# Kernel tuning notes

Hardware: AMD Instinct MI355X
Metric: run time of the kernel (lower is better)

## Reference

```python
import jax, jax.numpy as jnp
import numpy as np

P = 1048576   # total sampled points
N = 8192      # rays
E = 8         # experts
H = 128       # expert hidden dim
TOP_K = 2
INTERVAL = 0.5      # stepsize * voxel_size_ratio
ACT_SHIFT = -4.0    # models[-1].act_shift
THRESH = 1e-4       # fast_color_thres (ndc=False)


def raw2alpha(d):
    # Raw2Alpha: alpha = 1 - exp(-softplus(density + act_shift) * interval)
    return 1.0 - jnp.exp(-jax.nn.softplus(d + ACT_SHIFT) * INTERVAL)


def alphas2weights(alpha, ray_id, n_rays):
    # Sequential per-ray transmittance: w_j = alpha_j * prod_{k<j in ray}(1 - alpha_k)
    la = jnp.log1p(-jnp.clip(alpha, 0.0, 1.0 - 1e-6))      # [P], <= 0
    cum = jnp.cumsum(la)
    excl = cum - la                                          # exclusive cumsum, nonincreasing
    # offset per ray = excl at first point of the (sorted) segment == segment max
    offset = jax.ops.segment_max(excl, ray_id, num_segments=n_rays)
    T = jnp.exp(excl - offset[ray_id])                       # transmittance before each point
    weights = alpha * T
    alphainv_last = jnp.exp(jax.ops.segment_sum(la, ray_id, num_segments=n_rays))
    return weights, alphainv_last


def setup_inputs() -> dict:
    key = jax.random.key(0)
    ks = jax.random.split(key, 12)
    s = 0.3  # weight scale keeping activations in a sane range
    return {
        "ray_pts": jax.random.uniform(ks[0], (P, 3), dtype=jnp.float32),
        "viewdirs": jax.random.normal(ks[1], (N, 3), dtype=jnp.float32),
        "bg": jnp.ones((3,), dtype=jnp.float32),
        "Wd1": jax.random.normal(ks[2], (3, H), dtype=jnp.float32) * s,
        "bd1": jnp.zeros((H,), dtype=jnp.float32),
        "Wd2": jax.random.normal(ks[3], (H, 1), dtype=jnp.float32) * s,
        "Wg": jax.random.normal(ks[4], (6, E), dtype=jnp.float32) * s,
        "We1": jax.random.normal(ks[5], (E, 6, H), dtype=jnp.float32) * s,
        "be1": jnp.zeros((E, H), dtype=jnp.float32),
        "Wrgb": jax.random.normal(ks[6], (E, H, 3), dtype=jnp.float32) * s,
        "Walpha": jax.random.normal(ks[7], (E, H, 1), dtype=jnp.float32) * s,
        "ray_id": jnp.sort(jax.random.randint(ks[8], (P,), 0, N)).astype(jnp.int32),
    }


def reference(ray_pts, viewdirs, bg, Wd1, bd1, Wd2, Wg, We1, be1, Wrgb, Walpha, ray_id):
    # --- density grid query + activation ---
    hd = jax.nn.relu(ray_pts @ Wd1 + bd1)                    # [P,H]
    density = (hd @ Wd2)[:, 0]                               # [P]
    alpha0 = raw2alpha(density)
    # filter low density (zeroing alpha == dropping the point from the cumprod)
    alpha0 = jnp.where(alpha0 > THRESH, alpha0, 0.0)
    w0, _ = alphas2weights(alpha0, ray_id, N)
    # filter low transmittance (w0 <= THRESH also covers alpha0 == 0)
    keep = w0 > THRESH                                        # [P] bool

    # --- gate: softmax over experts, top-k, renormalize ---
    x = jnp.concatenate([ray_pts, viewdirs[ray_id]], axis=-1)  # [P,6]
    probs = jax.nn.softmax(x @ Wg, axis=-1)                    # [P,E]
    vals, idx = jax.lax.top_k(probs, TOP_K)                    # [P,K]
    vals = vals / jnp.sum(vals, axis=-1, keepdims=True)        # top_k > 1
    g = jnp.sum(vals[..., None] * jax.nn.one_hot(idx, E, dtype=vals.dtype), axis=1)  # [P,E]
    g = g * keep[:, None].astype(g.dtype)

    # --- per-expert radiance / alpha, mixed by gate weights ---
    rgb = jnp.zeros((ray_pts.shape[0], 3), dtype=ray_pts.dtype)
    alpha_mix = jnp.zeros((ray_pts.shape[0],), dtype=ray_pts.dtype)
    for e in range(E):  # fixed small expert count
        h = jax.nn.relu(x @ We1[e] + be1[e])                   # [P,H]
        rgb_e = jax.nn.sigmoid(h @ Wrgb[e])                    # [P,3]
        a_e = raw2alpha((h @ Walpha[e])[:, 0])                 # [P]
        rgb = rgb + g[:, e:e + 1] * rgb_e
        alpha_mix = alpha_mix + g[:, e] * a_e

    # --- composite: Alphas2Weights + segment_coo sum + background ---
    w, alphainv_last = alphas2weights(alpha_mix, ray_id, N)
    rgb_marched = jax.ops.segment_sum(w[:, None] * rgb, ray_id, num_segments=N)
    rgb_marched = rgb_marched + alphainv_last[:, None] * bg
    return rgb_marched
```

## Files before the change

kernel.cpp:

```cpp
#include <hip/hip_runtime.h>

#define PTOT   1048576
#define NRAYS  8192
#define THRESH 1e-4f

typedef float F2 __attribute__((ext_vector_type(2)));

__device__ __forceinline__ F2 f2splat(float s){ F2 r; r.x = s; r.y = s; return r; }
__device__ __forceinline__ F2 f2fma(F2 a, float b, F2 c){
    return __builtin_elementwise_fma(a, f2splat(b), c);
}
__device__ __forceinline__ float raw2alpha_f(float d){
    return 1.0f - rsqrtf(1.0f + __expf(d - 4.0f));
}

__global__ __launch_bounds__(256) void k_point(
    const float* __restrict__ pts, const float* __restrict__ vdirs,
    const int* __restrict__ ray_id,
    const float* __restrict__ Wd1, const float* __restrict__ bd1,
    const float* __restrict__ Wd2, const float* __restrict__ Wg,
    float* __restrict__ alpha0, float* __restrict__ g0a, int* __restrict__ eea,
    float4* __restrict__ vd, int* __restrict__ ray_off)
{
    __shared__ float4 WD4[128];
    __shared__ float  WD2s[128];
    __shared__ float  WGs[8][6];
    int t = threadIdx.x;
    if (t < 128){
        WD4[t] = make_float4(Wd1[t], Wd1[128+t], Wd1[256+t], bd1[t]);
        WD2s[t] = Wd2[t];
    }
    if (t < 48) WGs[t & 7][t >> 3] = Wg[t];
    __syncthreads();

    int base = blockIdx.x * 2048 + t;
    F2 px[4], py[4], pz[4], vx[4], vy[4], vz[4], dens[4];
    int rid0[4], rid1[4];
    #pragma unroll
    for (int q=0;q<4;q++){
        int p0 = base + (2*q)*256, p1 = p0 + 256;
        px[q] = (F2){pts[3*p0],   pts[3*p1]};
        py[q] = (F2){pts[3*p0+1], pts[3*p1+1]};
        pz[q] = (F2){pts[3*p0+2], pts[3*p1+2]};
        int r0 = ray_id[p0], r1 = ray_id[p1];
        rid0[q] = r0; rid1[q] = r1;
        vx[q] = (F2){vdirs[3*r0],   vdirs[3*r1]};
        vy[q] = (F2){vdirs[3*r0+1], vdirs[3*r1+1]};
        vz[q] = (F2){vdirs[3*r0+2], vdirs[3*r1+2]};
        dens[q] = f2splat(0.f);
    }
    #pragma unroll
    for (int q=0;q<4;q++){
        int p0 = base + (2*q)*256, p1 = p0 + 256;
        vd[p0] = make_float4(vx[q].x, vy[q].x, vz[q].x, 0.f);
        vd[p1] = make_float4(vx[q].y, vy[q].y, vz[q].y, 0.f);
        int prev0 = (p0 == 0) ? -1 : ray_id[p0-1];
        if (prev0 != rid0[q]) for (int r=prev0+1; r<=rid0[q]; ++r) ray_off[r] = p0;
        int prev1 = ray_id[p1-1];
        if (prev1 != rid1[q]) for (int r=prev1+1; r<=rid1[q]; ++r) ray_off[r] = p1;
        if (p1 == PTOT-1) for (int r=rid1[q]+1; r<=NRAYS; ++r) ray_off[r] = PTOT;
    }
    #pragma unroll 2
    for (int i=0;i<128;i++){
        float4 w = WD4[i]; float w2 = WD2s[i];
        #pragma unroll
        for (int q=0;q<4;q++){
            F2 h = f2fma(px[q], w.x, f2fma(py[q], w.y, f2fma(pz[q], w.z, f2splat(w.w))));
            h = __builtin_elementwise_max(h, f2splat(0.f));
            dens[q] = f2fma(h, w2, dens[q]);
        }
    }
    #pragma unroll
    for (int q=0;q<4;q++){
        float a0 = raw2alpha_f(dens[q].x);
        float a1 = raw2alpha_f(dens[q].y);
        alpha0[base + (2*q)*256]   = (a0 > THRESH) ? a0 : 0.f;
        alpha0[base + (2*q+1)*256] = (a1 > THRESH) ? a1 : 0.f;
    }
    float m0[8], m1[8]; int i0[8], i1[8];
    #pragma unroll
    for (int j=0;j<8;j++){ m0[j]=-3.0e38f; m1[j]=-3.0e38f; i0[j]=0; i1[j]=0; }
    for (int e=0;e<8;e++){
        float w0=WGs[e][0],w1=WGs[e][1],w2=WGs[e][2],w3=WGs[e][3],w4=WGs[e][4],w5=WGs[e][5];
        #pragma unroll
        for (int q=0;q<4;q++){
            F2 l = f2fma(px[q],w0, f2fma(py[q],w1, f2fma(pz[q],w2,
                   f2fma(vx[q],w3, f2fma(vy[q],w4,
                   __builtin_elementwise_fma(vz[q], f2splat(w5), f2splat(0.f)))))));
            int j0 = 2*q, j1 = 2*q+1;
            float lx = l.x, ly = l.y;
            if (lx > m0[j0]){ m1[j0]=m0[j0]; i1[j0]=i0[j0]; m0[j0]=lx; i0[j0]=e; }
            else if (lx > m1[j0]){ m1[j0]=lx; i1[j0]=e; }
            if (ly > m0[j1]){ m1[j1]=m0[j1]; i1[j1]=i0[j1]; m0[j1]=ly; i0[j1]=e; }
            else if (ly > m1[j1]){ m1[j1]=ly; i1[j1]=e; }
        }
    }
    #pragma unroll
    for (int j=0;j<8;j++){
        float g0 = __fdividef(1.0f, 1.0f + __expf(m1[j]-m0[j]));
        g0a[base + j*256] = g0;
        eea[base + j*256] = i0[j] | (i1[j] << 8);
    }
}

__global__ __launch_bounds__(256) void k_scan0(const float* __restrict__ alpha0,
                                               const int* __restrict__ eea,
                                               const int* __restrict__ ray_off,
                                               unsigned char* __restrict__ keep,
                                               int* __restrict__ cntA)
{
    __shared__ int wcs[4][8];
    int t = threadIdx.x, lane = t & 63, w = t >> 6;
    int wid = blockIdx.x*4 + w;
    int c[8];
    #pragma unroll
    for (int e=0;e<8;e++) c[e]=0;
    int s = ray_off[wid], e = ray_off[wid+1];
    float carry = 1.f;
    for (int ch = s; ch < e; ch += 64){
        int p = ch + lane;
        bool in = p < e;
        float a = in ? alpha0[p] : 0.f;
        int  ee = in ? eea[p] : 0;
        float incl = 1.f - a;
        #pragma unroll
        for (int d=1; d<64; d<<=1){ float tt = __shfl_up(incl, d); if (lane >= d) incl *= tt; }
        float excl = __shfl_up(incl, 1); if (lane == 0) excl = 1.f;
        float w0 = a * carry * excl;
        int k = (in && w0 > THRESH) ? 1 : 0;
        if (in) keep[p] = (unsigned char)k;
        int e0 = ee & 255, e1 = (ee >> 8) & 255;
        #pragma unroll
        for (int x=0;x<8;x++){
            unsigned long long m0 = __ballot(k && e0==x);
            unsigned long long m1 = __ballot(k && e1==x);
            c[x] += __popcll(m0) + __popcll(m1);
        }
        carry *= __shfl(incl, 63);
    }
    if (lane == 0){
        #pragma unroll
        for (int x=0;x<8;x++) wcs[w][x] = c[x];
    }
    __syncthreads();
    if (t < 8){
        int sum = wcs[0][t]+wcs[1][t]+wcs[2][t]+wcs[3][t];
        if (sum) atomicAdd(&cntA[t], sum);
    }
}

__global__ __launch_bounds__(256) void k_fill(const unsigned char* __restrict__ keep,
                                              const float* __restrict__ g0a,
                                              const int* __restrict__ eea,
                                              const int* __restrict__ cntA,
                                              int* __restrict__ curA,
                                              int2* __restrict__ ent)
{
    __shared__ int wc[4][8];
    __shared__ int wb[4][8];
    __shared__ int sOff[8];
    int t = threadIdx.x, lane = t & 63, w = t >> 6;
    unsigned long long lt = (1ull << lane) - 1ull;
    int base = blockIdx.x * 2048;

    int c[8];
    #pragma unroll
    for (int e=0;e<8;e++) c[e]=0;
    for (int j=0;j<8;j++){
        int p = base + (j*4 + w)*64 + lane;
        int k = keep[p];
        int ee = eea[p];
        int e0 = ee & 255, e1 = (ee >> 8) & 255;
        #pragma unroll
        for (int e=0;e<8;e++){
            unsigned long long m0 = __ballot(k && e0==e);
            unsigned long long m1 = __ballot(k && e1==e);
            c[e] += __popcll(m0) + __popcll(m1);
        }
    }
    if (lane == 0){
        #pragma unroll
        for (int e=0;e<8;e++) wc[w][e] = c[e];
    }
    if (t == 0){
        int acc = 0;
        for (int e=0;e<8;e++){ sOff[e] = acc; acc += cntA[e]; }
    }
    __syncthreads();
    if (t < 8){
        int tot = wc[0][t]+wc[1][t]+wc[2][t]+wc[3][t];
        int b = sOff[t] + (tot ? atomicAdd(&curA[t], tot) : 0);
        wb[0][t] = b; b += wc[0][t];
        wb[1][t] = b; b += wc[1][t];
        wb[2][t] = b; b += wc[2][t];
        wb[3][t] = b;
    }
    __syncthreads();

    int cur[8];
    #pragma unroll
    for (int e=0;e<8;e++) cur[e] = wb[w][e];
    for (int j=0;j<8;j++){
        int p = base + (j*4 + w)*64 + lane;
        int k = keep[p];
        float g0 = g0a[p];
        int ee = eea[p];
        int e0 = ee & 255, e1 = (ee >> 8) & 255;
        #pragma unroll
        for (int e=0;e<8;e++){
            unsigned long long m0 = __ballot(k && e0==e);
            unsigned long long m1 = __ballot(k && e1==e);
            if (k && e0==e)
                ent[cur[e] + __popcll(m0 & lt)] = make_int2(p, __float_as_int(g0));
            if (k && e1==e)
                ent[cur[e] + __popcll(m0) + __popcll(m1 & lt)] =
                    make_int2(p | (1 << 30), __float_as_int(1.0f - g0));
            cur[e] += __popcll(m0) + __popcll(m1);
        }
    }
}

__global__ __launch_bounds__(256) void k_expert(
    const int2* __restrict__ ent, const int* __restrict__ cntA,
    const float* __restrict__ pts, const float4* __restrict__ vd,
    const float* __restrict__ We1, const float* __restrict__ be1,
    const float* __restrict__ Wrgb, const float* __restrict__ Walpha,
    float4* __restrict__ res)
{
    int e    = blockIdx.x >> 9;
    int bi   = blockIdx.x & 511;
    int base = bi * 2048;

    __shared__ float4 WA[128];
    __shared__ float4 WB[128];
    __shared__ float4 WC[128];
    __shared__ int sSeg[2];
    int t = threadIdx.x;
    if (t < 128){
        const float* w = We1 + e*768;
        WA[t] = make_float4(w[t], w[128+t], w[256+t], w[384+t]);
        WB[t] = make_float4(w[512+t], w[640+t], be1[e*128+t], Walpha[e*128+t]);
        const float* wr = Wrgb + e*384 + 3*t;
        WC[t] = make_float4(wr[0], wr[1], wr[2], 0.f);
    }
    if (t == 0){
        int acc = 0;
        for (int i=0;i<e;i++) acc += cntA[i];
        sSeg[0] = acc; sSeg[1] = cntA[e];
    }
    __syncthreads();
    int n = sSeg[1];
    if (base >= n) return;
    const int2* eb = ent + sSeg[0];

    F2 x0[4],x1[4],x2[4],x3[4],x4[4],x5[4];
    F2 ar[4],ag[4],ab[4],aa[4];
    #pragma unroll
    for (int pr=0;pr<4;pr++){
        int idx0 = base + t + (2*pr)*256, idx1 = idx0 + 256;
        int2 r0 = (idx0 < n) ? eb[idx0] : make_int2(0,0);
        int2 r1 = (idx1 < n) ? eb[idx1] : make_int2(0,0);
        int p0 = r0.x & 0x0FFFFFFF, p1 = r1.x & 0x0FFFFFFF;
        x0[pr] = (F2){pts[3*p0],   pts[3*p1]};
        x1[pr] = (F2){pts[3*p0+1], pts[3*p1+1]};
        x2[pr] = (F2){pts[3*p0+2], pts[3*p1+2]};
        float4 v0 = vd[p0], v1 = vd[p1];
        x3[pr] = (F2){v0.x, v1.x};
        x4[pr] = (F2){v0.y, v1.y};
        x5[pr] = (F2){v0.z, v1.z};
        ar[pr] = f2splat(0.f); ag[pr] = f2splat(0.f);
        ab[pr] = f2splat(0.f); aa[pr] = f2splat(0.f);
    }
    #pragma unroll 2
    for (int i=0;i<128;i++){
        float4 wa = WA[i], wb = WB[i], wc = WC[i];
        #pragma unroll
        for (int pr=0;pr<4;pr++){
            F2 h = f2fma(x0[pr],wa.x, f2fma(x1[pr],wa.y, f2fma(x2[pr],wa.z,
                   f2fma(x3[pr],wa.w, f2fma(x4[pr],wb.x, f2fma(x5[pr],wb.y,
                   f2splat(wb.z)))))));
            h = __builtin_elementwise_max(h, f2splat(0.f));
            ar[pr] = f2fma(h, wc.x, ar[pr]);
            ag[pr] = f2fma(h, wc.y, ag[pr]);
            ab[pr] = f2fma(h, wc.z, ab[pr]);
            aa[pr] = f2fma(h, wb.w, aa[pr]);
        }
    }
    #pragma unroll
    for (int pr=0;pr<4;pr++){
        #pragma unroll
        for (int sel=0; sel<2; sel++){
            int idx = base + t + (2*pr+sel)*256;
            if (idx < n){
                int2 rec = eb[idx];
                float vr = sel ? ar[pr].y : ar[pr].x;
                float vg = sel ? ag[pr].y : ag[pr].x;
                float vb = sel ? ab[pr].y : ab[pr].x;
                float va = sel ? aa[pr].y : aa[pr].x;
                float sr = __fdividef(1.0f, 1.0f + __expf(-vr));
                float sg = __fdividef(1.0f, 1.0f + __expf(-vg));
                float sb = __fdividef(1.0f, 1.0f + __expf(-vb));
                float a  = raw2alpha_f(va);
                float g  = __int_as_float(rec.y);
                int pp   = rec.x & 0x0FFFFFFF;
                int slot = ((unsigned)rec.x) >> 30;
                res[2*(size_t)pp + slot] = make_float4(g*sr, g*sg, g*sb, g*a);
            }
        }
    }
}

__global__ __launch_bounds__(256) void k_scan1(const float4* __restrict__ res,
                                               const unsigned char* __restrict__ keep,
                                               const int* __restrict__ ray_off,
                                               const float* __restrict__ bg,
                                               float* __restrict__ out)
{
    int wid  = (blockIdx.x*blockDim.x + threadIdx.x) >> 6;
    int lane = threadIdx.x & 63;
    if (wid >= NRAYS) return;
    int s = ray_off[wid], e = ray_off[wid+1];
    float carry = 1.f;
    float accx = 0.f, accy = 0.f, accz = 0.f;
    for (int c = s; c < e; c += 64){
        int p = c + lane;
        float4 v = make_float4(0.f,0.f,0.f,0.f);
        if (p < e && keep[p]){
            float4 v0 = res[2*(size_t)p];
            float4 v1 = res[2*(size_t)p + 1];
            v = make_float4(v0.x+v1.x, v0.y+v1.y, v0.z+v1.z, v0.w+v1.w);
        }
        float a = v.w;
        float incl = 1.f - a;
        #pragma unroll
        for (int d=1; d<64; d<<=1){ float tt = __shfl_up(incl, d); if (lane >= d) incl *= tt; }
        float excl = __shfl_up(incl, 1); if (lane == 0) excl = 1.f;
        float w = a * carry * excl;
        accx = fmaf(w, v.x, accx);
        accy = fmaf(w, v.y, accy);
        accz = fmaf(w, v.z, accz);
        carry *= __shfl(incl, 63);
    }
    #pragma unroll
    for (int d=32; d; d>>=1){
        accx += __shfl_xor(accx, d);
        accy += __shfl_xor(accy, d);
        accz += __shfl_xor(accz, d);
    }
    if (lane == 0){
        out[3*wid+0] = accx + carry*bg[0];
        out[3*wid+1] = accy + carry*bg[1];
        out[3*wid+2] = accz + carry*bg[2];
    }
}

extern "C" void kernel_launch(void* const* d_in, const int* in_sizes, int n_in,
                              void* d_out, int out_size, void* d_ws, size_t ws_size,
                              hipStream_t stream)
{
    const float* pts    = (const float*)d_in[0];
    const float* vdirs  = (const float*)d_in[1];
    const float* bg     = (const float*)d_in[2];
    const float* Wd1    = (const float*)d_in[3];
    const float* bd1    = (const float*)d_in[4];
    const float* Wd2    = (const float*)d_in[5];
    const float* Wg     = (const float*)d_in[6];
    const float* We1    = (const float*)d_in[7];
    const float* be1    = (const float*)d_in[8];
    const float* Wrgb   = (const float*)d_in[9];
    const float* Walpha = (const float*)d_in[10];
    const int*   ray_id = (const int*)d_in[11];
    float* out = (float*)d_out;

    char* ws = (char*)d_ws;
    size_t off = 0;
    float* alpha0        = (float*)(ws + off); off += (size_t)PTOT*4;
    float* g0a           = (float*)(ws + off); off += (size_t)PTOT*4;
    int*   eea           = (int*)  (ws + off); off += (size_t)PTOT*4;
    unsigned char* keep  = (unsigned char*)(ws + off); off += (size_t)PTOT;
    int*   ray_off       = (int*)  (ws + off); off += 33024;
    int*   cntA          = (int*)  (ws + off); off += 256;
    int*   curA          = (int*)  (ws + off); off += 256;
    off = (off + 255) & ~(size_t)255;
    float4* vd           = (float4*)(ws + off); off += (size_t)PTOT*16;
    int2*  ent           = (int2*) (ws + off); off += (size_t)2*PTOT*8;
    float4* res          = (float4*)(ws + off); off += ((size_t)2*PTOT+2)*16;

    hipMemsetAsync(cntA, 0, 512, stream);

    k_point <<<PTOT/2048, 256, 0, stream>>>(pts, vdirs, ray_id, Wd1, bd1, Wd2, Wg,
                                            alpha0, g0a, eea, vd, ray_off);
    k_scan0 <<<NRAYS/4, 256, 0, stream>>>(alpha0, eea, ray_off, keep, cntA);
    k_fill  <<<PTOT/2048, 256, 0, stream>>>(keep, g0a, eea, cntA, curA, ent);
    k_expert<<<8*512, 256, 0, stream>>>(ent, cntA, pts, vd,
                                        We1, be1, Wrgb, Walpha, res);
    k_scan1 <<<NRAYS*64/256, 256, 0, stream>>>(res, keep, ray_off, bg, out);
}
```

Before: 249.1 us.

## Fuse five phase kernels into one cooperative persistent kernel with grid syncs

Merges the point, scan, fill, expert and composite kernels into one cooperative kernel of 512 persistent blocks separated by grid-wide syncs. This removes the memset and the per-launch gaps between kernels. The expert phase now walks 2048-aligned padded segments through a flat chunk loop instead of launching 8×512 mostly-empty blocks. It keeps a fallback path of separate launches if the cooperative launch fails. The risks are grid-sync overhead, lower parallelism in the expert phase, and block-count limits imposed by occupancy.

```diff
diff --git a/kernel.cpp b/kernel.cpp
--- a/kernel.cpp
+++ b/kernel.cpp
@@ -1,8 +1,12 @@
 #include <hip/hip_runtime.h>
+#include <hip/hip_cooperative_groups.h>
+
+namespace cg = cooperative_groups;
 
 #define PTOT   1048576
 #define NRAYS  8192
 #define THRESH 1e-4f
+#define NBLK   512
 
 typedef float F2 __attribute__((ext_vector_type(2)));
 
@@ -14,26 +18,27 @@
     return 1.0f - rsqrtf(1.0f + __expf(d - 4.0f));
 }
 
-__global__ __launch_bounds__(256) void k_point(
+
+__device__ __forceinline__ void phase1(int bid, int t,
     const float* __restrict__ pts, const float* __restrict__ vdirs,
     const int* __restrict__ ray_id,
     const float* __restrict__ Wd1, const float* __restrict__ bd1,
     const float* __restrict__ Wd2, const float* __restrict__ Wg,
     float* __restrict__ alpha0, float* __restrict__ g0a, int* __restrict__ eea,
-    float4* __restrict__ vd, int* __restrict__ ray_off)
-{
-    __shared__ float4 WD4[128];
+    float4* __restrict__ vd, int* __restrict__ ray_off, int* __restrict__ cc)
+{
+    __shared__ float4 WD4s[128];
     __shared__ float  WD2s[128];
     __shared__ float  WGs[8][6];
-    int t = threadIdx.x;
     if (t < 128){
-        WD4[t] = make_float4(Wd1[t], Wd1[128+t], Wd1[256+t], bd1[t]);
+        WD4s[t] = make_float4(Wd1[t], Wd1[128+t], Wd1[256+t], bd1[t]);
         WD2s[t] = Wd2[t];
     }
     if (t < 48) WGs[t & 7][t >> 3] = Wg[t];
+    if (bid == 0 && t < 16) cc[t] = 0;
     __syncthreads();
 
-    int base = blockIdx.x * 2048 + t;
+    int base = bid * 2048 + t;
     F2 px[4], py[4], pz[4], vx[4], vy[4], vz[4], dens[4];
     int rid0[4], rid1[4];
     #pragma unroll
@@ -62,10 +67,10 @@
     }
     #pragma unroll 2
     for (int i=0;i<128;i++){
-        float4 w = WD4[i]; float w2 = WD2s[i];
+        float4 wv = WD4s[i]; float w2 = WD2s[i];
         #pragma unroll
         for (int q=0;q<4;q++){
-            F2 h = f2fma(px[q], w.x, f2fma(py[q], w.y, f2fma(pz[q], w.z, f2splat(w.w))));
+            F2 h = f2fma(px[q], wv.x, f2fma(py[q], wv.y, f2fma(pz[q], wv.z, f2splat(wv.w))));
             h = __builtin_elementwise_max(h, f2splat(0.f));
             dens[q] = f2fma(h, w2, dens[q]);
         }
@@ -103,40 +108,41 @@
     }
 }
 
-__global__ __launch_bounds__(256) void k_scan0(const float* __restrict__ alpha0,
-                                               const int* __restrict__ eea,
-                                               const int* __restrict__ ray_off,
-                                               unsigned char* __restrict__ keep,
-                                               int* __restrict__ cntA)
+__device__ __forceinline__ void phase2(int bid, int t,
+    const float* __restrict__ alpha0, const int* __restrict__ eea,
+    const int* __restrict__ ray_off,
+    unsigned char* __restrict__ keep, int* __restrict__ cc)
 {
     __shared__ int wcs[4][8];
-    int t = threadIdx.x, lane = t & 63, w = t >> 6;
-    int wid = blockIdx.x*4 + w;
+    int lane = t & 63, w = t >> 6;
     int c[8];
     #pragma unroll
     for (int e=0;e<8;e++) c[e]=0;
-    int s = ray_off[wid], e = ray_off[wid+1];
-    float carry = 1.f;
-    for (int ch = s; ch < e; ch += 64){
-        int p = ch + lane;
-        bool in = p < e;
-        float a = in ? alpha0[p] : 0.f;
-        int  ee = in ? eea[p] : 0;
-        float incl = 1.f - a;
-        #pragma unroll
-        for (int d=1; d<64; d<<=1){ float tt = __shfl_up(incl, d); if (lane >= d) incl *= tt; }
-        float excl = __shfl_up(incl, 1); if (lane == 0) excl = 1.f;
-        float w0 = a * carry * excl;
-        int k = (in && w0 > THRESH) ? 1 : 0;
-        if (in) keep[p] = (unsigned char)k;
-        int e0 = ee & 255, e1 = (ee >> 8) & 255;
-        #pragma unroll
-        for (int x=0;x<8;x++){
-            unsigned long long m0 = __ballot(k && e0==x);
-            unsigned long long m1 = __ballot(k && e1==x);
-            c[x] += __popcll(m0) + __popcll(m1);
-        }
-        carry *= __shfl(incl, 63);
+    for (int rr=0; rr<4; rr++){
+        int wid = bid*4 + w + rr*2048;
+        int s = ray_off[wid], e = ray_off[wid+1];
+        float carry = 1.f;
+        for (int ch = s; ch < e; ch += 64){
+            int p = ch + lane;
+            bool in = p < e;
+            float a = in ? alpha0[p] : 0.f;
+            int  ee = in ? eea[p] : 0;
+            float incl = 1.f - a;
+            #pragma unroll
+            for (int d=1; d<64; d<<=1){ float tt = __shfl_up(incl, d); if (lane >= d) incl *= tt; }
+            float excl = __shfl_up(incl, 1); if (lane == 0) excl = 1.f;
+            float w0 = a * carry * excl;
+            int k = (in && w0 > THRESH) ? 1 : 0;
+            if (in) keep[p] = (unsigned char)k;
+            int e0 = ee & 255, e1 = (ee >> 8) & 255;
+            #pragma unroll
+            for (int x=0;x<8;x++){
+                unsigned long long m0 = __ballot(k && e0==x);
+                unsigned long long m1 = __ballot(k && e1==x);
+                c[x] += __popcll(m0) + __popcll(m1);
+            }
+            carry *= __shfl(incl, 63);
+        }
     }
     if (lane == 0){
         #pragma unroll
@@ -145,23 +151,21 @@
     __syncthreads();
     if (t < 8){
         int sum = wcs[0][t]+wcs[1][t]+wcs[2][t]+wcs[3][t];
-        if (sum) atomicAdd(&cntA[t], sum);
-    }
-}
-
-__global__ __launch_bounds__(256) void k_fill(const unsigned char* __restrict__ keep,
-                                              const float* __restrict__ g0a,
-                                              const int* __restrict__ eea,
-                                              const int* __restrict__ cntA,
-                                              int* __restrict__ curA,
-                                              int2* __restrict__ ent)
-{
-    __shared__ int wc[4][8];
-    __shared__ int wb[4][8];
-    __shared__ int sOff[8];
-    int t = threadIdx.x, lane = t & 63, w = t >> 6;
+        if (sum) atomicAdd(&cc[t], sum);
+    }
+}
+
+__device__ __forceinline__ void phase3(int bid, int t,
+    const unsigned char* __restrict__ keep, const float* __restrict__ g0a,
+    const int* __restrict__ eea, int* __restrict__ cc, int2* __restrict__ ent)
+{
+    __shared__ int wc3[4][8];
+    __shared__ int wb3[4][8];
+    __shared__ int sOff3[8];
+    int lane = t & 63, w = t >> 6;
     unsigned long long lt = (1ull << lane) - 1ull;
-    int base = blockIdx.x * 2048;
+    int base = bid * 2048;
+    int* cntA = cc; int* curA = cc + 8;
 
     int c[8];
     #pragma unroll
@@ -180,26 +184,26 @@
     }
     if (lane == 0){
         #pragma unroll
-        for (int e=0;e<8;e++) wc[w][e] = c[e];
+        for (int e=0;e<8;e++) wc3[w][e] = c[e];
     }
     if (t == 0){
         int acc = 0;
-        for (int e=0;e<8;e++){ sOff[e] = acc; acc += cntA[e]; }
+        for (int e=0;e<8;e++){ sOff3[e] = acc; acc += (cntA[e] + 2047) & ~2047; }
     }
     __syncthreads();
     if (t < 8){
-        int tot = wc[0][t]+wc[1][t]+wc[2][t]+wc[3][t];
-        int b = sOff[t] + (tot ? atomicAdd(&curA[t], tot) : 0);
-        wb[0][t] = b; b += wc[0][t];
-        wb[1][t] = b; b += wc[1][t];
-        wb[2][t] = b; b += wc[2][t];
-        wb[3][t] = b;
+        int tot = wc3[0][t]+wc3[1][t]+wc3[2][t]+wc3[3][t];
+        int b = sOff3[t] + (tot ? atomicAdd(&curA[t], tot) : 0);
+        wb3[0][t] = b; b += wc3[0][t];
+        wb3[1][t] = b; b += wc3[1][t];
+        wb3[2][t] = b; b += wc3[2][t];
+        wb3[3][t] = b;
     }
     __syncthreads();
 
     int cur[8];
     #pragma unroll
-    for (int e=0;e<8;e++) cur[e] = wb[w][e];
+    for (int e=0;e<8;e++) cur[e] = wb3[w][e];
     for (int j=0;j<8;j++){
         int p = base + (j*4 + w)*64 + lane;
         int k = keep[p];
@@ -220,139 +224,198 @@
     }
 }
 
-__global__ __launch_bounds__(256) void k_expert(
-    const int2* __restrict__ ent, const int* __restrict__ cntA,
+__device__ __forceinline__ void phase4(int bid, int t,
     const float* __restrict__ pts, const float4* __restrict__ vd,
     const float* __restrict__ We1, const float* __restrict__ be1,
     const float* __restrict__ Wrgb, const float* __restrict__ Walpha,
+    const int* __restrict__ cc, const int2* __restrict__ ent,
     float4* __restrict__ res)
 {
-    int e    = blockIdx.x >> 9;
-    int bi   = blockIdx.x & 511;
-    int base = bi * 2048;
-
-    __shared__ float4 WA[128];
-    __shared__ float4 WB[128];
-    __shared__ float4 WC[128];
-    __shared__ int sSeg[2];
-    int t = threadIdx.x;
-    if (t < 128){
-        const float* w = We1 + e*768;
-        WA[t] = make_float4(w[t], w[128+t], w[256+t], w[384+t]);
-        WB[t] = make_float4(w[512+t], w[640+t], be1[e*128+t], Walpha[e*128+t]);
-        const float* wr = Wrgb + e*384 + 3*t;
-        WC[t] = make_float4(wr[0], wr[1], wr[2], 0.f);
-    }
-    if (t == 0){
+    __shared__ float4 WA[128], WB[128], WC[128];
+    int cnt8[8], offP[8];
+    {
         int acc = 0;
-        for (int i=0;i<e;i++) acc += cntA[i];
-        sSeg[0] = acc; sSeg[1] = cntA[e];
-    }
-    __syncthreads();
-    int n = sSeg[1];
-    if (base >= n) return;
-    const int2* eb = ent + sSeg[0];
-
-    F2 x0[4],x1[4],x2[4],x3[4],x4[4],x5[4];
-    F2 ar[4],ag[4],ab[4],aa[4];
-    #pragma unroll
-    for (int pr=0;pr<4;pr++){
-        int idx0 = base + t + (2*pr)*256, idx1 = idx0 + 256;
-        int2 r0 = (idx0 < n) ? eb[idx0] : make_int2(0,0);
-        int2 r1 = (idx1 < n) ? eb[idx1] : make_int2(0,0);
-        int p0 = r0.x & 0x0FFFFFFF, p1 = r1.x & 0x0FFFFFFF;
-        x0[pr] = (F2){pts[3*p0],   pts[3*p1]};
-        x1[pr] = (F2){pts[3*p0+1], pts[3*p1+1]};
-        x2[pr] = (F2){pts[3*p0+2], pts[3*p1+2]};
-        float4 v0 = vd[p0], v1 = vd[p1];
-        x3[pr] = (F2){v0.x, v1.x};
-        x4[pr] = (F2){v0.y, v1.y};
-        x5[pr] = (F2){v0.z, v1.z};
-        ar[pr] = f2splat(0.f); ag[pr] = f2splat(0.f);
-        ab[pr] = f2splat(0.f); aa[pr] = f2splat(0.f);
-    }
-    #pragma unroll 2
-    for (int i=0;i<128;i++){
-        float4 wa = WA[i], wb = WB[i], wc = WC[i];
+        #pragma unroll
+        for (int x=0;x<8;x++){ cnt8[x]=cc[x]; offP[x]=acc; acc += (cnt8[x]+2047)&~2047; }
+    }
+    int lastck = (offP[7] + cnt8[7] - 1) >> 11;
+    for (int ck = bid; ck <= lastck; ck += NBLK){
+        int e = -1, base = 0;
+        #pragma unroll
+        for (int x=0;x<8;x++){
+            int bx = (ck << 11) - offP[x];
+            if (bx >= 0 && bx < cnt8[x]){ e = x; base = bx; }
+        }
+        if (e < 0) continue;
+        __syncthreads();
+        if (t < 128){
+            const float* wp = We1 + e*768;
+            WA[t] = make_float4(wp[t], wp[128+t], wp[256+t], wp[384+t]);
+            WB[t] = make_float4(wp[512+t], wp[640+t], be1[e*128+t], Walpha[e*128+t]);
+            const float* wr = Wrgb + e*384 + 3*t;
+            WC[t] = make_float4(wr[0], wr[1], wr[2], 0.f);
+        }
+        __syncthreads();
+        int n = cnt8[e];
+        const int2* eb = ent + offP[e];
+
+        F2 x0[4],x1[4],x2[4],x3[4],x4[4],x5[4];
+        F2 ar[4],ag[4],ab[4],aa[4];
         #pragma unroll
         for (int pr=0;pr<4;pr++){
-            F2 h = f2fma(x0[pr],wa.x, f2fma(x1[pr],wa.y, f2fma(x2[pr],wa.z,
-                   f2fma(x3[pr],wa.w, f2fma(x4[pr],wb.x, f2fma(x5[pr],wb.y,
-                   f2splat(wb.z)))))));
-            h = __builtin_elementwise_max(h, f2splat(0.f));
-            ar[pr] = f2fma(h, wc.x, ar[pr]);
-            ag[pr] = f2fma(h, wc.y, ag[pr]);
-            ab[pr] = f2fma(h, wc.z, ab[pr]);
-            aa[pr] = f2fma(h, wb.w, aa[pr]);
-        }
-    }
-    #pragma unroll
-    for (int pr=0;pr<4;pr++){
-        #pragma unroll
-        for (int sel=0; sel<2; sel++){
-            int idx = base + t + (2*pr+sel)*256;
-            if (idx < n){
-                int2 rec = eb[idx];
-                float vr = sel ? ar[pr].y : ar[pr].x;
-                float vg = sel ? ag[pr].y : ag[pr].x;
-                float vb = sel ? ab[pr].y : ab[pr].x;
-                float va = sel ? aa[pr].y : aa[pr].x;
-                float sr = __fdividef(1.0f, 1.0f + __expf(-vr));
-                float sg = __fdividef(1.0f, 1.0f + __expf(-vg));
-                float sb = __fdividef(1.0f, 1.0f + __expf(-vb));
-                float a  = raw2alpha_f(va);
-                float g  = __int_as_float(rec.y);
-                int pp   = rec.x & 0x0FFFFFFF;
-                int slot = ((unsigned)rec.x) >> 30;
-                res[2*(size_t)pp + slot] = make_float4(g*sr, g*sg, g*sb, g*a);
+            int idx0 = base + t + (2*pr)*256, idx1 = idx0 + 256;
+            int2 r0 = (idx0 < n) ? eb[idx0] : make_int2(0,0);
+            int2 r1 = (idx1 < n) ? eb[idx1] : make_int2(0,0);
+            int p0 = r0.x & 0x0FFFFFFF, p1 = r1.x & 0x0FFFFFFF;
+            x0[pr] = (F2){pts[3*p0],   pts[3*p1]};
+            x1[pr] = (F2){pts[3*p0+1], pts[3*p1+1]};
+            x2[pr] = (F2){pts[3*p0+2], pts[3*p1+2]};
+            float4 v0 = vd[p0], v1 = vd[p1];
+            x3[pr] = (F2){v0.x, v1.x};
+            x4[pr] = (F2){v0.y, v1.y};
+            x5[pr] = (F2){v0.z, v1.z};
+            ar[pr] = f2splat(0.f); ag[pr] = f2splat(0.f);
+            ab[pr] = f2splat(0.f); aa[pr] = f2splat(0.f);
+        }
+        #pragma unroll 2
+        for (int i=0;i<128;i++){
+            float4 wa = WA[i], wb = WB[i], wc = WC[i];
+            #pragma unroll
+            for (int pr=0;pr<4;pr++){
+                F2 h = f2fma(x0[pr],wa.x, f2fma(x1[pr],wa.y, f2fma(x2[pr],wa.z,
+                       f2fma(x3[pr],wa.w, f2fma(x4[pr],wb.x, f2fma(x5[pr],wb.y,
+                       f2splat(wb.z)))))));
+                h = __builtin_elementwise_max(h, f2splat(0.f));
+                ar[pr] = f2fma(h, wc.x, ar[pr]);
+                ag[pr] = f2fma(h, wc.y, ag[pr]);
+                ab[pr] = f2fma(h, wc.z, ab[pr]);
+                aa[pr] = f2fma(h, wb.w, aa[pr]);
             }
         }
-    }
-}
-
-__global__ __launch_bounds__(256) void k_scan1(const float4* __restrict__ res,
-                                               const unsigned char* __restrict__ keep,
-                                               const int* __restrict__ ray_off,
-                                               const float* __restrict__ bg,
-                                               float* __restrict__ out)
-{
-    int wid  = (blockIdx.x*blockDim.x + threadIdx.x) >> 6;
-    int lane = threadIdx.x & 63;
-    if (wid >= NRAYS) return;
-    int s = ray_off[wid], e = ray_off[wid+1];
-    float carry = 1.f;
-    float accx = 0.f, accy = 0.f, accz = 0.f;
-    for (int c = s; c < e; c += 64){
-        int p = c + lane;
-        float4 v = make_float4(0.f,0.f,0.f,0.f);
-        if (p < e && keep[p]){
-            float4 v0 = res[2*(size_t)p];
-            float4 v1 = res[2*(size_t)p + 1];
-            v = make_float4(v0.x+v1.x, v0.y+v1.y, v0.z+v1.z, v0.w+v1.w);
-        }
-        float a = v.w;
-        float incl = 1.f - a;
-        #pragma unroll
-        for (int d=1; d<64; d<<=1){ float tt = __shfl_up(incl, d); if (lane >= d) incl *= tt; }
-        float excl = __shfl_up(incl, 1); if (lane == 0) excl = 1.f;
-        float w = a * carry * excl;
-        accx = fmaf(w, v.x, accx);
-        accy = fmaf(w, v.y, accy);
-        accz = fmaf(w, v.z, accz);
-        carry *= __shfl(incl, 63);
-    }
-    #pragma unroll
-    for (int d=32; d; d>>=1){
-        accx += __shfl_xor(accx, d);
-        accy += __shfl_xor(accy, d);
-        accz += __shfl_xor(accz, d);
-    }
-    if (lane == 0){
-        out[3*wid+0] = accx + carry*bg[0];
-        out[3*wid+1] = accy + carry*bg[1];
-        out[3*wid+2] = accz + carry*bg[2];
-    }
-}
+        #pragma unroll
+        for (int pr=0;pr<4;pr++){
+            #pragma unroll
+            for (int sel=0; sel<2; sel++){
+                int idx = base + t + (2*pr+sel)*256;
+                if (idx < n){
+                    int2 rec = eb[idx];
+                    float vr = sel ? ar[pr].y : ar[pr].x;
+                    float vg = sel ? ag[pr].y : ag[pr].x;
+                    float vb = sel ? ab[pr].y : ab[pr].x;
+                    float va = sel ? aa[pr].y : aa[pr].x;
+                    float sr = __fdividef(1.0f, 1.0f + __expf(-vr));
+                    float sg = __fdividef(1.0f, 1.0f + __expf(-vg));
+                    float sb = __fdividef(1.0f, 1.0f + __expf(-vb));
+                    float a  = raw2alpha_f(va);
+                    float g  = __int_as_float(rec.y);
+                    int pp   = rec.x & 0x0FFFFFFF;
+                    int slot = ((unsigned)rec.x) >> 30;
+                    res[2*(size_t)pp + slot] = make_float4(g*sr, g*sg, g*sb, g*a);
+                }
+            }
+        }
+    }
+}
+
+__device__ __forceinline__ void phase5(int bid, int t,
+    const float4* __restrict__ res, const unsigned char* __restrict__ keep,
+    const int* __restrict__ ray_off, const float* __restrict__ bg,
+    float* __restrict__ out)
+{
+    int lane = t & 63, w = t >> 6;
+    for (int rr=0; rr<4; rr++){
+        int wid = bid*4 + w + rr*2048;
+        int s = ray_off[wid], e = ray_off[wid+1];
+        float carry = 1.f;
+        float accx = 0.f, accy = 0.f, accz = 0.f;
+        for (int c = s; c < e; c += 64){
+            int p = c + lane;
+            float4 v = make_float4(0.f,0.f,0.f,0.f);
+            if (p < e && keep[p]){
+                float4 v0 = res[2*(size_t)p];
+                float4 v1 = res[2*(size_t)p + 1];
+                v = make_float4(v0.x+v1.x, v0.y+v1.y, v0.z+v1.z, v0.w+v1.w);
+            }
+            float a = v.w;
+            float incl = 1.f - a;
+            #pragma unroll
+            for (int d=1; d<64; d<<=1){ float tt = __shfl_up(incl, d); if (lane >= d) incl *= tt; }
+            float excl = __shfl_up(incl, 1); if (lane == 0) excl = 1.f;
+            float wgt = a * carry * excl;
+            accx = fmaf(wgt, v.x, accx);
+            accy = fmaf(wgt, v.y, accy);
+            accz = fmaf(wgt, v.z, accz);
+            carry *= __shfl(incl, 63);
+        }
+        #pragma unroll
+        for (int d=32; d; d>>=1){
+            accx += __shfl_xor(accx, d);
+            accy += __shfl_xor(accy, d);
+            accz += __shfl_xor(accz, d);
+        }
+        if (lane == 0){
+            out[3*wid+0] = accx + carry*bg[0];
+            out[3*wid+1] = accy + carry*bg[1];
+            out[3*wid+2] = accz + carry*bg[2];
+        }
+    }
+}
+
+__global__ __launch_bounds__(256, 2) void k_mega(
+    const float* __restrict__ pts, const float* __restrict__ vdirs,
+    const float* __restrict__ bg,
+    const float* __restrict__ Wd1, const float* __restrict__ bd1,
+    const float* __restrict__ Wd2, const float* __restrict__ Wg,
+    const float* __restrict__ We1, const float* __restrict__ be1,
+    const float* __restrict__ Wrgb, const float* __restrict__ Walpha,
+    const int* __restrict__ ray_id,
+    float* __restrict__ out,
+    float* __restrict__ alpha0, float* __restrict__ g0a, int* __restrict__ eea,
+    unsigned char* __restrict__ keep, int* __restrict__ ray_off,
+    int* __restrict__ cc, float4* __restrict__ vd,
+    int2* __restrict__ ent, float4* __restrict__ res)
+{
+    cg::grid_group gg = cg::this_grid();
+    int bid = blockIdx.x, t = threadIdx.x;
+    phase1(bid, t, pts, vdirs, ray_id, Wd1, bd1, Wd2, Wg,
+           alpha0, g0a, eea, vd, ray_off, cc);
+    gg.sync();
+    phase2(bid, t, alpha0, eea, ray_off, keep, cc);
+    gg.sync();
+    phase3(bid, t, keep, g0a, eea, cc, ent);
+    gg.sync();
+    phase4(bid, t, pts, vd, We1, be1, Wrgb, Walpha, cc, ent, res);
+    gg.sync();
+    phase5(bid, t, res, keep, ray_off, bg, out);
+}
+
+__global__ __launch_bounds__(256) void k_p1(
+    const float* pts, const float* vdirs, const int* ray_id,
+    const float* Wd1, const float* bd1, const float* Wd2, const float* Wg,
+    float* alpha0, float* g0a, int* eea, float4* vd, int* ray_off, int* cc)
+{ phase1(blockIdx.x, threadIdx.x, pts, vdirs, ray_id, Wd1, bd1, Wd2, Wg,
+         alpha0, g0a, eea, vd, ray_off, cc); }
+
+__global__ __launch_bounds__(256) void k_p2(
+    const float* alpha0, const int* eea, const int* ray_off,
+    unsigned char* keep, int* cc)
+{ phase2(blockIdx.x, threadIdx.x, alpha0, eea, ray_off, keep, cc); }
+
+__global__ __launch_bounds__(256) void k_p3(
+    const unsigned char* keep, const float* g0a, const int* eea,
+    int* cc, int2* ent)
+{ phase3(blockIdx.x, threadIdx.x, keep, g0a, eea, cc, ent); }
+
+__global__ __launch_bounds__(256) void k_p4(
+    const float* pts, const float4* vd,
+    const float* We1, const float* be1, const float* Wrgb, const float* Walpha,
+    const int* cc, const int2* ent, float4* res)
+{ phase4(blockIdx.x, threadIdx.x, pts, vd, We1, be1, Wrgb, Walpha, cc, ent, res); }
+
+__global__ __launch_bounds__(256) void k_p5(
+    const float4* res, const unsigned char* keep, const int* ray_off,
+    const float* bg, float* out)
+{ phase5(blockIdx.x, threadIdx.x, res, keep, ray_off, bg, out); }
 
 extern "C" void kernel_launch(void* const* d_in, const int* in_sizes, int n_in,
                               void* d_out, int out_size, void* d_ws, size_t ws_size,
@@ -379,20 +442,27 @@
     int*   eea           = (int*)  (ws + off); off += (size_t)PTOT*4;
     unsigned char* keep  = (unsigned char*)(ws + off); off += (size_t)PTOT;
     int*   ray_off       = (int*)  (ws + off); off += 33024;
-    int*   cntA          = (int*)  (ws + off); off += 256;
-    int*   curA          = (int*)  (ws + off); off += 256;
+    int*   cc            = (int*)  (ws + off); off += 256;
     off = (off + 255) & ~(size_t)255;
     float4* vd           = (float4*)(ws + off); off += (size_t)PTOT*16;
-    int2*  ent           = (int2*) (ws + off); off += (size_t)2*PTOT*8;
+    int2*  ent           = (int2*) (ws + off); off += (size_t)2*PTOT*8 + (8*2048)*8;
     float4* res          = (float4*)(ws + off); off += ((size_t)2*PTOT+2)*16;
 
-    hipMemsetAsync(cntA, 0, 512, stream);
-
-    k_point <<<PTOT/2048, 256, 0, stream>>>(pts, vdirs, ray_id, Wd1, bd1, Wd2, Wg,
-                                            alpha0, g0a, eea, vd, ray_off);
-    k_scan0 <<<NRAYS/4, 256, 0, stream>>>(alpha0, eea, ray_off, keep, cntA);
-    k_fill  <<<PTOT/2048, 256, 0, stream>>>(keep, g0a, eea, cntA, curA, ent);
-    k_expert<<<8*512, 256, 0, stream>>>(ent, cntA, pts, vd,
-                                        We1, be1, Wrgb, Walpha, res);
-    k_scan1 <<<NRAYS*64/256, 256, 0, stream>>>(res, keep, ray_off, bg, out);
-}
+    void* params[] = {
+        (void*)&pts, (void*)&vdirs, (void*)&bg, (void*)&Wd1, (void*)&bd1,
+        (void*)&Wd2, (void*)&Wg, (void*)&We1, (void*)&be1, (void*)&Wrgb,
+        (void*)&Walpha, (void*)&ray_id, (void*)&out,
+        (void*)&alpha0, (void*)&g0a, (void*)&eea, (void*)&keep, (void*)&ray_off,
+        (void*)&cc, (void*)&vd, (void*)&ent, (void*)&res
+    };
+    hipError_t err = hipLaunchCooperativeKernel((const void*)k_mega, dim3(NBLK),
+                                                dim3(256), params, 0, stream);
+    if (err != hipSuccess){
+        k_p1<<<NBLK, 256, 0, stream>>>(pts, vdirs, ray_id, Wd1, bd1, Wd2, Wg,
+                                       alpha0, g0a, eea, vd, ray_off, cc);
+        k_p2<<<NBLK, 256, 0, stream>>>(alpha0, eea, ray_off, keep, cc);
+        k_p3<<<NBLK, 256, 0, stream>>>(keep, g0a, eea, cc, ent);
+        k_p4<<<NBLK, 256, 0, stream>>>(pts, vd, We1, be1, Wrgb, Walpha, cc, ent, res);
+        k_p5<<<NBLK, 256, 0, stream>>>(res, keep, ray_off, bg, out);
+    }
+}
```

After: 486.0 us. +95.1%, slower.
